# Optimization experiments

Hardware: AMD Instinct MI355X
Metric: run time of the kernel (lower is better)

The kernel has to match this reference:

```python
import jax, jax.numpy as jnp
import numpy as np


def gcn_layer(x, src, dst, deg_inv_sqrt, W, b):
    # PyG GCNConv: h = X W; out[i] = sum_{j->i} norm(j,i) * h[j] + deg_i^{-1} * h[i] + b
    n = x.shape[0]
    h = x @ W                                   # [N, out]
    norm = deg_inv_sqrt[src] * deg_inv_sqrt[dst]  # [E]
    msg = h[src] * norm[:, None]                # [E, out]
    agg = jax.ops.segment_sum(msg, dst, num_segments=n)
    # self-loop contribution (added loops with norm = deg_i^{-1})
    agg = agg + h * (deg_inv_sqrt * deg_inv_sqrt)[:, None]
    return agg + b


def setup_inputs() -> dict:
    key = jax.random.key(0)
    k1, k2, k3, k4, k5, k6 = jax.random.split(key, 6)
    N, E, IN, HID, OUT = 50000, 800000, 128, 128, 64
    x = jax.random.normal(k1, (N, IN), dtype=jnp.float32)
    edge_index = jax.random.randint(k2, (2, E), 0, N, dtype=jnp.int64)
    # glorot-ish init for weights, zeros-ish bias
    W1 = jax.random.normal(k3, (IN, HID), dtype=jnp.float32) * (1.0 / np.sqrt(IN))
    b1 = jax.random.normal(k4, (HID,), dtype=jnp.float32) * 0.01
    W2 = jax.random.normal(k5, (HID, OUT), dtype=jnp.float32) * (1.0 / np.sqrt(HID))
    b2 = jax.random.normal(k6, (OUT,), dtype=jnp.float32) * 0.01
    return {"x": x, "edge_index": edge_index, "W1": W1, "b1": b1, "W2": W2, "b2": b2}


def reference(x, edge_index, W1, b1, W2, b2):
    n = x.shape[0]
    src, dst = edge_index[0], edge_index[1]
    # degree with self-loops (PyG computes degree on the dst/col index)
    deg = jax.ops.segment_sum(jnp.ones_like(dst, dtype=x.dtype), dst, num_segments=n) + 1.0
    deg_inv_sqrt = jax.lax.rsqrt(deg)
    h = gcn_layer(x, src, dst, deg_inv_sqrt, W1, b1)
    h = jax.nn.relu(h)
    # F.dropout with training=False is identity (module evaluated in eval mode)
    out = gcn_layer(h, src, dst, deg_inv_sqrt, W2, b2)
    return out
```

## Files before the change

### kernel.cpp

```cpp
#include <hip/hip_runtime.h>
#include <stdint.h>

typedef __attribute__((ext_vector_type(8))) short short8;
typedef __attribute__((ext_vector_type(4))) float floatx4;

static inline size_t align256(size_t x) { return (x + 255) & ~size_t(255); }

__device__ __forceinline__ unsigned short f2bf(float f) {
    unsigned u = __float_as_uint(f);
    u += 0x7fff + ((u >> 16) & 1);
    return (unsigned short)(u >> 16);
}
__device__ __forceinline__ unsigned pack_bf16(float a, float b) {
    return (unsigned)f2bf(a) | ((unsigned)f2bf(b) << 16);
}
__device__ __forceinline__ float bf_lo(unsigned u) { return __uint_as_float(u << 16); }
__device__ __forceinline__ float bf_hi(unsigned u) { return __uint_as_float(u & 0xffff0000u); }

#define BSHIFT 7
#define NBMAX 1024
#define CH 2048
#define SCAP 3072

__device__ __forceinline__ bool detect_i32(const void* eidx, int E, int t) {
    const long long* e64 = (const long long*)eidx;
    int nchk = E < 256 ? E : 256;
    long long v = e64[t % nchk];
    int bad = (v < 0 || v > 0x7fffffffLL) ? 1 : 0;
    return __syncthreads_or(bad) != 0;
}

__global__ __launch_bounds__(256) void k_hist(const void* __restrict__ eidx, int E,
        int* __restrict__ chist, int NB, int NC,
        const float* __restrict__ W1, const float* __restrict__ W2,
        unsigned short* __restrict__ w1t, unsigned short* __restrict__ w2t,
        int K1, int M1, int K2, int M2) {
    __shared__ int hist[NBMAX];
    const int t = threadIdx.x, B = blockIdx.x;
    if (B < NC) {
        const int e0 = B * CH;
        const int e1 = (e0 + CH < E) ? e0 + CH : E;
        const bool i32 = detect_i32(eidx, E, t);
        const int* e32 = (const int*)eidx;
        const long long* e64 = (const long long*)eidx;
        for (int b0 = 0; b0 < NB; b0 += NBMAX) {
            int bw = (NB - b0 < NBMAX) ? NB - b0 : NBMAX;
            for (int i = t; i < bw; i += 256) hist[i] = 0;
            __syncthreads();
            for (int e = e0 + t; e < e1; e += 256) {
                int d = i32 ? e32[(size_t)E + e] : (int)e64[(size_t)E + e];
                int b = (d >> BSHIFT) - b0;
                if (b >= 0 && b < bw) atomicAdd(&hist[b], 1);
            }
            __syncthreads();
            for (int i = t; i < bw; i += 256) chist[(size_t)(b0 + i) * NC + B] = hist[i];
            __syncthreads();
        }
    } else if (B == NC) {
        for (int j = t; j < K1 * M1; j += 256) {
            int k = j / M1, n = j % M1;
            w1t[(size_t)n * K1 + k] = f2bf(W1[j]);
        }
    } else if (B == NC + 1) {
        for (int j = t; j < K2 * M2; j += 256) {
            int k = j / M2, n = j % M2;
            w2t[(size_t)n * K2 + k] = f2bf(W2[j]);
        }
    }
}

__global__ __launch_bounds__(256) void k_btot(const int* __restrict__ chist,
                                              int* __restrict__ btot, int NB, int NC) {
    int b = blockIdx.x * 4 + (threadIdx.x >> 6);
    if (b >= NB) return;
    int lane = threadIdx.x & 63;
    const int* row = chist + (size_t)b * NC;
    int v = 0;
    for (int i = lane; i < NC; i += 64) v += row[i];
    #pragma unroll
    for (int off = 32; off >= 1; off >>= 1) v += __shfl_xor(v, off, 64);
    if (lane == 0) btot[b] = v;
}

__global__ __launch_bounds__(1024) void k_bscan(const int* __restrict__ btot,
                                                int* __restrict__ bbase,
                                                int* __restrict__ rs_final,
                                                int NB, int N) {
    __shared__ int swt[16];
    const int t = threadIdx.x, lane = t & 63, w = t >> 6;
    int carry = 0;
    for (int base = 0; base < NB; base += 1024) {
        int i = base + t;
        int v = (i < NB) ? btot[i] : 0;
        int incl = v;
        #pragma unroll
        for (int off = 1; off < 64; off <<= 1) {
            int nbr = __shfl_up(incl, off, 64);
            if (lane >= off) incl += nbr;
        }
        if (lane == 63) swt[w] = incl;
        __syncthreads();
        int woff = 0;
        for (int j = 0; j < w; ++j) woff += swt[j];
        if (i < NB) bbase[i] = carry + woff + incl - v;
        int tot = 0;
        for (int j = 0; j < 16; ++j) tot += swt[j];
        carry += tot;
        __syncthreads();
    }
    if (t == 0) { bbase[NB] = carry; rs_final[N] = carry; }
}

__global__ __launch_bounds__(256) void k_hscan2(int* __restrict__ chist,
                                                const int* __restrict__ bbase,
                                                int NB, int NC) {
    int b = blockIdx.x * 4 + (threadIdx.x >> 6);
    if (b >= NB) return;
    int lane = threadIdx.x & 63;
    int* row = chist + (size_t)b * NC;
    int carry = bbase[b];
    for (int base = 0; base < NC; base += 64) {
        int i = base + lane;
        int v = (i < NC) ? row[i] : 0;
        int incl = v;
        #pragma unroll
        for (int off = 1; off < 64; off <<= 1) {
            int nbr = __shfl_up(incl, off, 64);
            if (lane >= off) incl += nbr;
        }
        if (i < NC) row[i] = carry + incl - v;
        carry += __shfl(incl, 63, 64);
    }
}

__global__ __launch_bounds__(256) void k_bfill(const void* __restrict__ eidx, int E,
                                               const int* __restrict__ chist,
                                               unsigned* __restrict__ bbuf, int NB, int NC) {
    __shared__ int rank[NBMAX];
    __shared__ int base[NBMAX];
    const int t = threadIdx.x, c = blockIdx.x;
    const int e0 = c * CH;
    const int e1 = (e0 + CH < E) ? e0 + CH : E;
    const bool i32 = detect_i32(eidx, E, t);
    const int* e32 = (const int*)eidx;
    const long long* e64 = (const long long*)eidx;
    for (int b0 = 0; b0 < NB; b0 += NBMAX) {
        int bw = (NB - b0 < NBMAX) ? NB - b0 : NBMAX;
        for (int i = t; i < bw; i += 256) {
            rank[i] = 0;
            base[i] = chist[(size_t)(b0 + i) * NC + c];
        }
        __syncthreads();
        for (int e = e0 + t; e < e1; e += 256) {
            int s, d;
            if (i32) { s = e32[e]; d = e32[(size_t)E + e]; }
            else     { s = (int)e64[e]; d = (int)e64[(size_t)E + e]; }
            int b = (d >> BSHIFT) - b0;
            if (b >= 0 && b < bw) {
                int slot = base[b] + atomicAdd(&rank[b], 1);
                bbuf[slot] = ((unsigned)(d & 127) << 25) | (unsigned)s;
            }
        }
        __syncthreads();
    }
}

__global__ __launch_bounds__(256) void k_sort(const unsigned* __restrict__ bbuf,
                                              const int* __restrict__ bbase,
                                              int* __restrict__ rs_final,
                                              float* __restrict__ dinv,
                                              int* __restrict__ esrc, int N) {
    __shared__ int hist[128];
    __shared__ int off[128];
    __shared__ int srcbuf[SCAP];
    const int b = blockIdx.x, t = threadIdx.x;
    const int node0 = b << BSHIFT;
    const int nloc = (N - node0 < 128) ? N - node0 : 128;
    const int s0 = bbase[b], s1 = bbase[b + 1];
    const int cnt = s1 - s0;
    if (t < 128) hist[t] = 0;
    __syncthreads();
    for (int i = s0 + t; i < s1; i += 256)
        atomicAdd(&hist[bbuf[i] >> 25], 1);
    __syncthreads();
    if (t < 64) {
        int carry = 0;
        #pragma unroll
        for (int base = 0; base < 128; base += 64) {
            int v = hist[base + t];
            int incl = v;
            #pragma unroll
            for (int o = 1; o < 64; o <<= 1) {
                int nbr = __shfl_up(incl, o, 64);
                if (t >= o) incl += nbr;
            }
            off[base + t] = carry + incl - v;
            carry += __shfl(incl, 63, 64);
        }
    }
    __syncthreads();
    if (t < nloc) {
        rs_final[node0 + t] = s0 + off[t];
        dinv[node0 + t] = rsqrtf((float)hist[t] + 1.0f);
    }
    __syncthreads();
    if (t < 128) hist[t] = 0;
    __syncthreads();
    if (cnt <= SCAP) {
        for (int i = s0 + t; i < s1; i += 256) {
            unsigned sd = bbuf[i];
            int lo = sd >> 25;
            int r = atomicAdd(&hist[lo], 1);
            srcbuf[off[lo] + r] = (int)(sd & 0x1ffffffu);
        }
        __syncthreads();
        for (int i = t; i < cnt; i += 256) esrc[s0 + i] = srcbuf[i];
    } else {
        for (int i = s0 + t; i < s1; i += 256) {
            unsigned sd = bbuf[i];
            int lo = sd >> 25;
            int r = atomicAdd(&hist[lo], 1);
            esrc[s0 + off[lo] + r] = (int)(sd & 0x1ffffffu);
        }
    }
}

template<int BN, bool AF32>
__global__ __launch_bounds__(256, 3) void k_gemm(
        const void* __restrict__ Av, const unsigned short* __restrict__ Bt,
        const float* __restrict__ dinv, unsigned short* __restrict__ C,
        int N, int M) {
    constexpr int LD = 136;
    __shared__ unsigned short As[64 * LD];
    __shared__ unsigned short Bs[BN * LD];
    const int tid = threadIdx.x;
    const int wave = tid >> 6, lane = tid & 63;
    const int q = lane >> 4, tm = lane & 15;
    const int row0 = blockIdx.x * 64;

    {
        const uint4* Bg = (const uint4*)Bt;
        #pragma unroll
        for (int it = 0; it < BN / 16; ++it) {
            int i = tid + it * 256;
            int r = i >> 4, o = i & 15;
            *(uint4*)&Bs[r * LD + o * 8] = Bg[(size_t)r * 16 + o];
        }
    }
    if (AF32) {
        const float4* Ag = (const float4*)Av;
        #pragma unroll
        for (int it = 0; it < 8; ++it) {
            int i = tid + it * 256;
            int r = i >> 5, o = i & 31;
            int row = row0 + r;
            float4 v = make_float4(0.f, 0.f, 0.f, 0.f);
            if (row < N) v = Ag[(size_t)row * 32 + o];
            uint2 pk;
            pk.x = pack_bf16(v.x, v.y);
            pk.y = pack_bf16(v.z, v.w);
            *(uint2*)&As[r * LD + o * 4] = pk;
        }
    } else {
        const uint4* Ag = (const uint4*)Av;
        #pragma unroll
        for (int it = 0; it < 4; ++it) {
            int i = tid + it * 256;
            int r = i >> 4, o = i & 15;
            int row = row0 + r;
            uint4 v = make_uint4(0, 0, 0, 0);
            if (row < N) v = Ag[(size_t)row * 16 + o];
            *(uint4*)&As[r * LD + o * 8] = v;
        }
    }
    __syncthreads();

    constexpr int NG = BN / 16;
    floatx4 acc[NG];
    #pragma unroll
    for (int g = 0; g < NG; ++g) acc[g] = (floatx4){0.f, 0.f, 0.f, 0.f};

    const int arow = wave * 16 + tm;
    #pragma unroll
    for (int kc = 0; kc < 4; ++kc) {
        short8 af = *(const short8*)&As[arow * LD + kc * 32 + q * 8];
        #pragma unroll
        for (int g = 0; g < NG; ++g) {
            short8 bf = *(const short8*)&Bs[(g * 16 + tm) * LD + kc * 32 + q * 8];
            acc[g] = __builtin_amdgcn_mfma_f32_16x16x32_bf16(af, bf, acc[g], 0, 0, 0);
        }
    }

    float dv[4];
    #pragma unroll
    for (int r = 0; r < 4; ++r) {
        int row = row0 + wave * 16 + q * 4 + r;
        dv[r] = (row < N) ? dinv[row] : 0.f;
    }
    #pragma unroll
    for (int g = 0; g < NG; ++g) {
        #pragma unroll
        for (int r = 0; r < 4; ++r) {
            int row = row0 + wave * 16 + q * 4 + r;
            if (row < N) C[(size_t)row * M + g * 16 + tm] = f2bf(dv[r] * acc[g][r]);
        }
    }
}

__global__ __launch_bounds__(256) void k_agg128(const unsigned* __restrict__ Hb,
        const float* __restrict__ dinv, const int* __restrict__ rs,
        const int* __restrict__ esrc, const float* __restrict__ bias,
        unsigned* __restrict__ out, int N) {
    int wid = (blockIdx.x * 256 + threadIdx.x) >> 6;
    if (wid >= N) return;
    int l = threadIdx.x & 63;
    float di = dinv[wid];
    unsigned a = Hb[(size_t)wid * 64 + l];
    float accx = bf_lo(a), accy = bf_hi(a);
    int k = rs[wid], kend = rs[wid + 1];
    for (; k + 8 <= kend; k += 8) {
        int s[8];
        #pragma unroll
        for (int j = 0; j < 8; ++j) s[j] = esrc[k + j];
        unsigned g[8];
        #pragma unroll
        for (int j = 0; j < 8; ++j) g[j] = Hb[(size_t)s[j] * 64 + l];
        #pragma unroll
        for (int j = 0; j < 8; ++j) { accx += bf_lo(g[j]); accy += bf_hi(g[j]); }
    }
    if (k + 4 <= kend) {
        int s[4];
        #pragma unroll
        for (int j = 0; j < 4; ++j) s[j] = esrc[k + j];
        unsigned g[4];
        #pragma unroll
        for (int j = 0; j < 4; ++j) g[j] = Hb[(size_t)s[j] * 64 + l];
        #pragma unroll
        for (int j = 0; j < 4; ++j) { accx += bf_lo(g[j]); accy += bf_hi(g[j]); }
        k += 4;
    }
    for (; k < kend; ++k) {
        unsigned g = Hb[(size_t)esrc[k] * 64 + l];
        accx += bf_lo(g); accy += bf_hi(g);
    }
    float2 b = ((const float2*)bias)[l];
    float ox = fmaxf(fmaf(di, accx, b.x), 0.f);
    float oy = fmaxf(fmaf(di, accy, b.y), 0.f);
    out[(size_t)wid * 64 + l] = pack_bf16(ox, oy);
}

__global__ __launch_bounds__(256) void k_agg64(const unsigned short* __restrict__ Hb,
        const float* __restrict__ dinv, const int* __restrict__ rs,
        const int* __restrict__ esrc, const float* __restrict__ bias,
        float* __restrict__ out, int N) {
    int wid = (blockIdx.x * 256 + threadIdx.x) >> 6;
    if (wid >= N) return;
    int l = threadIdx.x & 63;
    float di = dinv[wid];
    float acc = __uint_as_float((unsigned)Hb[(size_t)wid * 64 + l] << 16);
    int k = rs[wid], kend = rs[wid + 1];
    for (; k + 8 <= kend; k += 8) {
        int s[8];
        #pragma unroll
        for (int j = 0; j < 8; ++j) s[j] = esrc[k + j];
        unsigned short g[8];
        #pragma unroll
        for (int j = 0; j < 8; ++j) g[j] = Hb[(size_t)s[j] * 64 + l];
        #pragma unroll
        for (int j = 0; j < 8; ++j) acc += __uint_as_float((unsigned)g[j] << 16);
    }
    if (k + 4 <= kend) {
        int s[4];
        #pragma unroll
        for (int j = 0; j < 4; ++j) s[j] = esrc[k + j];
        unsigned short g[4];
        #pragma unroll
        for (int j = 0; j < 4; ++j) g[j] = Hb[(size_t)s[j] * 64 + l];
        #pragma unroll
        for (int j = 0; j < 4; ++j) acc += __uint_as_float((unsigned)g[j] << 16);
        k += 4;
    }
    for (; k < kend; ++k)
        acc += __uint_as_float((unsigned)Hb[(size_t)esrc[k] * 64 + l] << 16);
    out[(size_t)wid * 64 + l] = fmaf(di, acc, bias[l]);
}

extern "C" void kernel_launch(void* const* d_in, const int* in_sizes, int n_in,
                              void* d_out, int out_size, void* d_ws, size_t ws_size,
                              hipStream_t stream) {
    const float* x  = (const float*)d_in[0];
    const void*  ei = d_in[1];
    const float* W1 = (const float*)d_in[2];
    const float* b1 = (const float*)d_in[3];
    const float* W2 = (const float*)d_in[4];
    const float* b2 = (const float*)d_in[5];

    int HID = in_sizes[3];
    int IN  = in_sizes[2] / HID;
    int OUT = in_sizes[4] / HID;
    int N   = in_sizes[0] / IN;
    int E   = in_sizes[1] / 2;
    int NB  = (N + 127) >> BSHIFT;
    int NC  = (E + CH - 1) / CH;

    char* p = (char*)d_ws;
    int* chist     = (int*)p;   p += align256((size_t)NB * NC * 4);
    int* btot      = (int*)p;   p += align256((size_t)NB * 4);
    int* bbase     = (int*)p;   p += align256((size_t)(NB + 1) * 4);
    int* rs_final  = (int*)p;   p += align256((size_t)(N + 1) * 4);
    int* esrc      = (int*)p;   p += align256((size_t)E * 4);
    float* dinv    = (float*)p; p += align256((size_t)N * 4);
    unsigned short* w1t = (unsigned short*)p; p += align256((size_t)HID * IN * 2);
    unsigned short* w2t = (unsigned short*)p; p += align256((size_t)OUT * HID * 2);
    size_t hb_bytes = (size_t)N * HID * 2, bbuf_bytes = (size_t)E * 4;
    unsigned* bbuf = (unsigned*)p;
    unsigned short* hb = (unsigned short*)p;
    p += align256(hb_bytes > bbuf_bytes ? hb_bytes : bbuf_bytes);
    unsigned short* h1b = (unsigned short*)p; p += align256((size_t)N * HID * 2);
    unsigned short* h2b = (unsigned short*)p; p += align256((size_t)N * OUT * 2);

    k_hist<<<NC + 2, 256, 0, stream>>>(ei, E, chist, NB, NC,
                                       W1, W2, w1t, w2t, IN, HID, HID, OUT);
    k_btot<<<(NB + 3) / 4, 256, 0, stream>>>(chist, btot, NB, NC);
    k_bscan<<<1, 1024, 0, stream>>>(btot, bbase, rs_final, NB, N);
    k_hscan2<<<(NB + 3) / 4, 256, 0, stream>>>(chist, bbase, NB, NC);
    k_bfill<<<NC, 256, 0, stream>>>(ei, E, chist, bbuf, NB, NC);
    k_sort<<<NB, 256, 0, stream>>>(bbuf, bbase, rs_final, dinv, esrc, N);

    k_gemm<128, true><<<(N + 63) / 64, 256, 0, stream>>>(x, w1t, dinv, hb, N, HID);
    k_agg128<<<(N + 3) / 4, 256, 0, stream>>>((unsigned*)hb, dinv, rs_final, esrc, b1,
                                              (unsigned*)h1b, N);

    k_gemm<64, false><<<(N + 63) / 64, 256, 0, stream>>>(h1b, w2t, dinv, h2b, N, OUT);
    k_agg64<<<(N + 3) / 4, 256, 0, stream>>>(h2b, dinv, rs_final, esrc, b2, (float*)d_out, N);
}
```

Before: 205.8 us.

## Fuse layer-1 aggregation with layer-2 GEMM in one kernel

```diff
diff --git a/kernel.cpp b/kernel.cpp
--- a/kernel.cpp
+++ b/kernel.cpp
@@ -225,11 +225,11 @@
     }
 }
 
-template<int BN, bool AF32>
-__global__ __launch_bounds__(256, 3) void k_gemm(
-        const void* __restrict__ Av, const unsigned short* __restrict__ Bt,
+__global__ __launch_bounds__(256, 3) void k_gemm1(
+        const float* __restrict__ Av, const unsigned short* __restrict__ Bt,
         const float* __restrict__ dinv, unsigned short* __restrict__ C,
         int N, int M) {
+    constexpr int BN = 128;
     constexpr int LD = 136;
     __shared__ unsigned short As[64 * LD];
     __shared__ unsigned short Bs[BN * LD];
@@ -247,7 +247,7 @@
             *(uint4*)&Bs[r * LD + o * 8] = Bg[(size_t)r * 16 + o];
         }
     }
-    if (AF32) {
+    {
         const float4* Ag = (const float4*)Av;
         #pragma unroll
         for (int it = 0; it < 8; ++it) {
@@ -261,17 +261,6 @@
             pk.y = pack_bf16(v.z, v.w);
             *(uint2*)&As[r * LD + o * 4] = pk;
         }
-    } else {
-        const uint4* Ag = (const uint4*)Av;
-        #pragma unroll
-        for (int it = 0; it < 4; ++it) {
-            int i = tid + it * 256;
-            int r = i >> 4, o = i & 15;
-            int row = row0 + r;
-            uint4 v = make_uint4(0, 0, 0, 0);
-            if (row < N) v = Ag[(size_t)row * 16 + o];
-            *(uint4*)&As[r * LD + o * 8] = v;
-        }
     }
     __syncthreads();
 
@@ -307,46 +296,86 @@
     }
 }
 
-__global__ __launch_bounds__(256) void k_agg128(const unsigned* __restrict__ Hb,
+__global__ __launch_bounds__(256) void k_agg128g(const unsigned* __restrict__ Hb,
         const float* __restrict__ dinv, const int* __restrict__ rs,
         const int* __restrict__ esrc, const float* __restrict__ bias,
-        unsigned* __restrict__ out, int N) {
-    int wid = (blockIdx.x * 256 + threadIdx.x) >> 6;
-    if (wid >= N) return;
-    int l = threadIdx.x & 63;
-    float di = dinv[wid];
-    unsigned a = Hb[(size_t)wid * 64 + l];
-    float accx = bf_lo(a), accy = bf_hi(a);
-    int k = rs[wid], kend = rs[wid + 1];
-    for (; k + 8 <= kend; k += 8) {
-        int s[8];
-        #pragma unroll
-        for (int j = 0; j < 8; ++j) s[j] = esrc[k + j];
-        unsigned g[8];
-        #pragma unroll
-        for (int j = 0; j < 8; ++j) g[j] = Hb[(size_t)s[j] * 64 + l];
-        #pragma unroll
-        for (int j = 0; j < 8; ++j) { accx += bf_lo(g[j]); accy += bf_hi(g[j]); }
-    }
-    if (k + 4 <= kend) {
-        int s[4];
-        #pragma unroll
-        for (int j = 0; j < 4; ++j) s[j] = esrc[k + j];
-        unsigned g[4];
-        #pragma unroll
-        for (int j = 0; j < 4; ++j) g[j] = Hb[(size_t)s[j] * 64 + l];
-        #pragma unroll
-        for (int j = 0; j < 4; ++j) { accx += bf_lo(g[j]); accy += bf_hi(g[j]); }
-        k += 4;
-    }
-    for (; k < kend; ++k) {
-        unsigned g = Hb[(size_t)esrc[k] * 64 + l];
-        accx += bf_lo(g); accy += bf_hi(g);
-    }
-    float2 b = ((const float2*)bias)[l];
-    float ox = fmaxf(fmaf(di, accx, b.x), 0.f);
-    float oy = fmaxf(fmaf(di, accy, b.y), 0.f);
-    out[(size_t)wid * 64 + l] = pack_bf16(ox, oy);
+        const unsigned short* __restrict__ W2t,
+        unsigned short* __restrict__ h2b, int N) {
+    constexpr int LD = 136;
+    __shared__ unsigned short h1s[16 * LD];
+    __shared__ unsigned short w2s[64 * LD];
+    const int t = threadIdx.x;
+    const int wave = t >> 6, l = t & 63;
+    const int q = l >> 4, tm = l & 15;
+    const int node0 = blockIdx.x * 16;
+
+    {
+        const uint4* Wg = (const uint4*)W2t;
+        #pragma unroll
+        for (int it = 0; it < 4; ++it) {
+            int i = t + it * 256;
+            int r = i >> 4, o = i & 15;
+            *(uint4*)&w2s[r * LD + o * 8] = Wg[(size_t)r * 16 + o];
+        }
+    }
+
+    const float2 bv = ((const float2*)bias)[l];
+    #pragma unroll
+    for (int nn = 0; nn < 4; ++nn) {
+        int nloc = wave * 4 + nn;
+        int wid = node0 + nloc;
+        unsigned pk = 0;
+        if (wid < N) {
+            unsigned a = Hb[(size_t)wid * 64 + l];
+            float accx = bf_lo(a), accy = bf_hi(a);
+            int k = rs[wid], kend = rs[wid + 1];
+            for (; k + 8 <= kend; k += 8) {
+                int s[8];
+                #pragma unroll
+                for (int j = 0; j < 8; ++j) s[j] = esrc[k + j];
+                unsigned g[8];
+                #pragma unroll
+                for (int j = 0; j < 8; ++j) g[j] = Hb[(size_t)s[j] * 64 + l];
+                #pragma unroll
+                for (int j = 0; j < 8; ++j) { accx += bf_lo(g[j]); accy += bf_hi(g[j]); }
+            }
+            if (k + 4 <= kend) {
+                int s[4];
+                #pragma unroll
+                for (int j = 0; j < 4; ++j) s[j] = esrc[k + j];
+                unsigned g[4];
+                #pragma unroll
+                for (int j = 0; j < 4; ++j) g[j] = Hb[(size_t)s[j] * 64 + l];
+                #pragma unroll
+                for (int j = 0; j < 4; ++j) { accx += bf_lo(g[j]); accy += bf_hi(g[j]); }
+                k += 4;
+            }
+            for (; k < kend; ++k) {
+                unsigned g = Hb[(size_t)esrc[k] * 64 + l];
+                accx += bf_lo(g); accy += bf_hi(g);
+            }
+            float di = dinv[wid];
+            float ox = fmaxf(fmaf(di, accx, bv.x), 0.f);
+            float oy = fmaxf(fmaf(di, accy, bv.y), 0.f);
+            pk = pack_bf16(ox, oy);
+        }
+        *(unsigned*)&h1s[nloc * LD + 2 * l] = pk;
+    }
+    __syncthreads();
+
+    floatx4 acc = (floatx4){0.f, 0.f, 0.f, 0.f};
+    #pragma unroll
+    for (int kc = 0; kc < 4; ++kc) {
+        short8 af = *(const short8*)&h1s[tm * LD + kc * 32 + q * 8];
+        short8 bf = *(const short8*)&w2s[(wave * 16 + tm) * LD + kc * 32 + q * 8];
+        acc = __builtin_amdgcn_mfma_f32_16x16x32_bf16(af, bf, acc, 0, 0, 0);
+    }
+    #pragma unroll
+    for (int r = 0; r < 4; ++r) {
+        int node = node0 + q * 4 + r;
+        if (node < N)
+            h2b[(size_t)node * 64 + wave * 16 + tm] = f2bf(dinv[node] * acc[r]);
+    }
 }
 
 __global__ __launch_bounds__(256) void k_agg64(const unsigned short* __restrict__ Hb,
@@ -416,7 +445,6 @@
     unsigned* bbuf = (unsigned*)p;
     unsigned short* hb = (unsigned short*)p;
     p += align256(hb_bytes > bbuf_bytes ? hb_bytes : bbuf_bytes);
-    unsigned short* h1b = (unsigned short*)p; p += align256((size_t)N * HID * 2);
     unsigned short* h2b = (unsigned short*)p; p += align256((size_t)N * OUT * 2);
 
     k_hist<<<NC + 2, 256, 0, stream>>>(ei, E, chist, NB, NC,
@@ -427,10 +455,11 @@
     k_bfill<<<NC, 256, 0, stream>>>(ei, E, chist, bbuf, NB, NC);
     k_sort<<<NB, 256, 0, stream>>>(bbuf, bbase, rs_final, dinv, esrc, N);
 
-    k_gemm<128, true><<<(N + 63) / 64, 256, 0, stream>>>(x, w1t, dinv, hb, N, HID);
-    k_agg128<<<(N + 3) / 4, 256, 0, stream>>>((unsigned*)hb, dinv, rs_final, esrc, b1,
-                                              (unsigned*)h1b, N);
-
-    k_gemm<64, false><<<(N + 63) / 64, 256, 0, stream>>>(h1b, w2t, dinv, h2b, N, OUT);
-    k_agg64<<<(N + 3) / 4, 256, 0, stream>>>(h2b, dinv, rs_final, esrc, b2, (float*)d_out, N);
-}
+    k_gemm1<<<(N + 63) / 64, 256, 0, stream>>>(x, w1t, dinv, hb, N, HID);
+
+    k_agg128g<<<(N + 15) / 16, 256, 0, stream>>>((unsigned*)hb, dinv, rs_final, esrc,
+                                                 b1, w2t, h2b, N);
+
+    k_agg64<<<(N + 3) / 4, 256, 0, stream>>>(h2b, dinv, rs_final, esrc, b2,
+                                             (float*)d_out, N);
+}
```

Result: no change. 206.4 us (+0.3%).
